# Performance work log

Measured on AMD Instinct MI355X. Metric: run time of the kernel, lower is better.

The kernel has to match this reference:

```python
import jax, jax.numpy as jnp
import numpy as np

N_SLOTS = 64
DECAY = 0.999
B, S, H, M = 4, 4096, 2048, 128


def _l2norm(t, eps=1e-12):
    return t / jnp.maximum(jnp.linalg.norm(t, axis=-1, keepdims=True), eps)


def setup_inputs() -> dict:
    key = jax.random.key(0)
    ks = jax.random.split(key, 6)
    return {
        "x": jax.random.normal(ks[0], (B, S, H), dtype=jnp.float32),
        "W_query": jax.random.normal(ks[1], (M, H), dtype=jnp.float32) * 0.02,
        "W_key": jax.random.normal(ks[2], (M, H), dtype=jnp.float32) * 0.02,
        "W_value": jax.random.normal(ks[3], (M, H), dtype=jnp.float32) * 0.02,
        "W_out": jax.random.normal(ks[4], (H, M), dtype=jnp.float32) * 0.02,
        "W_gate_w": jax.random.normal(ks[5], (1, H), dtype=jnp.float32) * 0.02,
        "W_gate_b": jnp.full((1,), -2.0, dtype=jnp.float32),
        "log_beta": jnp.full((1,), np.log(8.0), dtype=jnp.float32),
        "chunk_size": 64,
    }


def reference(x, W_query, W_key, W_value, W_out, W_gate_w, W_gate_b, log_beta, chunk_size):
    b, s, h = x.shape
    m = W_query.shape[0]
    dt = x.dtype

    q = x @ W_query.T                      # (b, s, m)
    k = _l2norm(x @ W_key.T)               # (b, s, m)
    v = _l2norm(x @ W_value.T)             # (b, s, m)
    gate = jax.nn.sigmoid(x @ W_gate_w.T + W_gate_b)  # (b, s, 1)
    beta = jnp.exp(log_beta).reshape(())

    nc = s // chunk_size
    decay_c = jnp.asarray(DECAY, dt) ** chunk_size

    def chunkify(t):
        # (b, s, d) -> (nc, b, chunk, d)
        return jnp.moveaxis(t.reshape(b, nc, chunk_size, -1), 1, 0)

    qc, kc, vc = chunkify(q), chunkify(k), chunkify(v)
    wc = chunkify(gate)[..., 0]            # (nc, b, chunk)

    K0 = jnp.zeros((N_SLOTS, m), dt)
    V0 = jnp.zeros((N_SLOTS, m), dt)
    s0 = jnp.zeros((N_SLOTS,), dt)
    ptr0 = jnp.asarray(0, jnp.int32)

    def step(carry, inp):
        K_mem, V_mem, mem_strength, ptr = carry
        qch, kch, vch, wch = inp           # (b,c,m) x3, (b,c)
        # --- read: softmax retrieval over active slots ---
        slot_mask = (mem_strength > 1e-8).astype(dt)           # (n_slots,)
        scores = jnp.einsum("bcm,nm->bcn", qch, K_mem) * beta
        scores = scores + (1.0 - slot_mask) * -1e9
        attn = jax.nn.softmax(scores, axis=-1)
        r = jnp.einsum("bcn,nm->bcm", attn, V_mem)
        r = jnp.where(mem_strength.sum() < 1e-8, jnp.zeros_like(r), r)
        # --- write: gated aggregation into one slot ---
        w_sum = jnp.maximum(wch.sum(), 1e-8)
        k_agg = _l2norm((kch * wch[..., None]).sum((0, 1)) / w_sum)
        v_agg = _l2norm((vch * wch[..., None]).sum((0, 1)) / w_sum)
        write_str = wch.mean()
        mem_strength = mem_strength * decay_c
        slot = ptr % N_SLOTS
        K_mem = K_mem.at[slot].set(k_agg)
        V_mem = V_mem.at[slot].set(v_agg)
        mem_strength = mem_strength.at[slot].set(write_str)
        return (K_mem, V_mem, mem_strength, ptr + 1), (r, write_str)

    _, (rs, wss) = jax.lax.scan(step, (K0, V0, s0, ptr0), (qc, kc, vc, wc))

    retrieved = jnp.moveaxis(rs, 0, 1).reshape(b, s, m)
    out = retrieved @ W_out.T              # (b, s, h)
    # clamp output norm to 10
    onorm = jnp.maximum(jnp.linalg.norm(out, axis=-1, keepdims=True), 1e-6)
    out = out * jnp.minimum(10.0 / onorm, 1.0)
    mean_ws = jnp.mean(wss)
    return out, mean_ws
```

## Files before the change

kernel.cpp:

```cpp
#include <hip/hip_runtime.h>
#include <math.h>
#include <stdint.h>

#define NTOK 16384
#define SEQ  4096
#define HD   2048
#define MD   128
#define NCH  64
#define CHK  64

typedef __attribute__((ext_vector_type(8))) _Float16 half8;
typedef __attribute__((ext_vector_type(4))) float floatx4;

__device__ __forceinline__ void gload_lds16(const void* g, void* l) {
    __builtin_amdgcn_global_load_lds(
        (const __attribute__((address_space(1))) unsigned int*)(uintptr_t)g,
        (__attribute__((address_space(3))) unsigned int*)(uintptr_t)l,
        16, 0, 0);
}

__global__ __launch_bounds__(256) void convert_w_kernel(
    const float* __restrict__ Wq, const float* __restrict__ Wk,
    const float* __restrict__ Wv, const float* __restrict__ Wo,
    _Float16* __restrict__ Wcath, _Float16* __restrict__ Woh)
{
    int i = blockIdx.x * 256 + threadIdx.x;
    if (i < 384 * HD) {
        int r = i >> 11;
        float val;
        if (r < 128)      val = Wq[i];
        else if (r < 256) val = Wk[i - 128 * HD];
        else              val = Wv[i - 256 * HD];
        Wcath[i] = (_Float16)val;
    } else {
        int j = i - 384 * HD;
        Woh[j] = (_Float16)Wo[j];
    }
}

__global__ __launch_bounds__(128) void gmat_kernel(
    const float* __restrict__ Wo, float* __restrict__ G)
{
    __shared__ float col[HD];
    int a = blockIdx.x;
    int b = threadIdx.x;
    for (int j = b; j < HD; j += 128) col[j] = Wo[(size_t)j * MD + a];
    __syncthreads();
    float s = 0.f;
    for (int j = 0; j < HD; ++j) s = fmaf(col[j], Wo[(size_t)j * MD + b], s);
    G[a * MD + b] = s;
}

__global__ __launch_bounds__(256, 3) void gemm_proj_mfma(
    const float* __restrict__ x, const _Float16* __restrict__ Wcath,
    const float* __restrict__ Wgw, const float* __restrict__ gb,
    float* __restrict__ q, float* __restrict__ k, float* __restrict__ v,
    float* __restrict__ wg)
{
    __shared__ _Float16 As[2][64 * 64];
    __shared__ _Float16 Bs[2][128 * 64];
    floatx4 acc[2][4];
    #pragma unroll
    for (int i = 0; i < 2; ++i)
        #pragma unroll
        for (int j = 0; j < 4; ++j) acc[i][j] = (floatx4){0.f, 0.f, 0.f, 0.f};

    const int tid  = threadIdx.x;
    const int wave = tid >> 6, lane = tid & 63;
    const int wm = wave & 1, wn = wave >> 1;
    const int row0 = blockIdx.x * 64;
    const int col0 = blockIdx.y * 128;
    const bool do_gate = (blockIdx.y == 0);

    const int ar0 = tid >> 3;
    const int ac0 = (tid & 7) ^ (ar0 & 7);
    const float* xA0 = x + (size_t)(row0 + ar0) * HD + ac0 * 8;
    const float* xA1 = x + (size_t)(row0 + ar0 + 32) * HD + ac0 * 8;
    const float* wgp = Wgw + ac0 * 8;

    float gacc0 = 0.f, gacc1 = 0.f;
    float4 a00, a01, a10, a11, g0, g1;

#define STAGE_B(buf_, k0_) do {                                               \
        _Pragma("unroll")                                                     \
        for (int rnd = 0; rnd < 4; ++rnd) {                                   \
            int sg = rnd * 4 + wave;                                          \
            int br = sg * 8 + (lane >> 3);                                    \
            int bc = (lane & 7) ^ (br & 7);                                   \
            gload_lds16(Wcath + (size_t)(col0 + br) * HD + (k0_) + bc * 8,    \
                        (char*)Bs[buf_] + sg * 1024);                         \
        } } while (0)

#define LOAD_A(k0_) do {                                                      \
        a00 = *(const float4*)(xA0 + (k0_));                                  \
        a01 = *(const float4*)(xA0 + (k0_) + 4);                              \
        a10 = *(const float4*)(xA1 + (k0_));                                  \
        a11 = *(const float4*)(xA1 + (k0_) + 4);                              \
        if (do_gate) {                                                        \
            g0 = *(const float4*)(wgp + (k0_));                               \
            g1 = *(const float4*)(wgp + (k0_) + 4);                           \
        } } while (0)

#define FINISH_A(buf_) do {                                                   \
        if (do_gate) {                                                        \
            gacc0 += a00.x*g0.x + a00.y*g0.y + a00.z*g0.z + a00.w*g0.w        \
                   + a01.x*g1.x + a01.y*g1.y + a01.z*g1.z + a01.w*g1.w;       \
            gacc1 += a10.x*g0.x + a10.y*g0.y + a10.z*g0.z + a10.w*g0.w        \
                   + a11.x*g1.x + a11.y*g1.y + a11.z*g1.z + a11.w*g1.w;       \
        }                                                                     \
        half8 h0, h1;                                                         \
        h0[0] = (_Float16)a00.x; h0[1] = (_Float16)a00.y;                     \
        h0[2] = (_Float16)a00.z; h0[3] = (_Float16)a00.w;                     \
        h0[4] = (_Float16)a01.x; h0[5] = (_Float16)a01.y;                     \
        h0[6] = (_Float16)a01.z; h0[7] = (_Float16)a01.w;                     \
        h1[0] = (_Float16)a10.x; h1[1] = (_Float16)a10.y;                     \
        h1[2] = (_Float16)a10.z; h1[3] = (_Float16)a10.w;                     \
        h1[4] = (_Float16)a11.x; h1[5] = (_Float16)a11.y;                     \
        h1[6] = (_Float16)a11.z; h1[7] = (_Float16)a11.w;                     \
        *(half8*)((char*)As[buf_] + tid * 16)        = h0;                    \
        *(half8*)((char*)As[buf_] + 4096 + tid * 16) = h1;                    \
    } while (0)

#define COMPUTE(buf_) do {                                                    \
        half8 af[2][2], bf[4][2];                                             \
        _Pragma("unroll")                                                     \
        for (int i = 0; i < 2; ++i) {                                         \
            int r  = wm * 32 + i * 16 + (lane & 15);                          \
            int rb = r * 128 + (lane >> 4) * 16;                              \
            int sw = (r & 7) << 4;                                            \
            af[i][0] = *(const half8*)((const char*)As[buf_] + ( rb       ^ sw)); \
            af[i][1] = *(const half8*)((const char*)As[buf_] + ((rb + 64) ^ sw)); \
        }                                                                     \
        _Pragma("unroll")                                                     \
        for (int j = 0; j < 4; ++j) {                                         \
            int r  = wn * 64 + j * 16 + (lane & 15);                          \
            int rb = r * 128 + (lane >> 4) * 16;                              \
            int sw = (r & 7) << 4;                                            \
            bf[j][0] = *(const half8*)((const char*)Bs[buf_] + ( rb       ^ sw)); \
            bf[j][1] = *(const half8*)((const char*)Bs[buf_] + ((rb + 64) ^ sw)); \
        }                                                                     \
        _Pragma("unroll")                                                     \
        for (int ks = 0; ks < 2; ++ks)                                        \
            _Pragma("unroll")                                                 \
            for (int i = 0; i < 2; ++i)                                       \
                _Pragma("unroll")                                             \
                for (int j = 0; j < 4; ++j)                                   \
                    acc[i][j] = __builtin_amdgcn_mfma_f32_16x16x32_f16(       \
                        af[i][ks], bf[j][ks], acc[i][j], 0, 0, 0);            \
    } while (0)

    STAGE_B(0, 0);
    LOAD_A(0);
    FINISH_A(0);
    __syncthreads();

    int cur = 0;
    for (int t = 0; t < HD / 64; ++t) {
        if (t < HD / 64 - 1) {
            STAGE_B(cur ^ 1, (t + 1) * 64);
            LOAD_A((t + 1) * 64);
        }
        COMPUTE(cur);
        if (t < HD / 64 - 1) FINISH_A(cur ^ 1);
        __syncthreads();
        cur ^= 1;
    }

    if (do_gate) {
        gacc0 += __shfl_xor(gacc0, 1);
        gacc0 += __shfl_xor(gacc0, 2);
        gacc0 += __shfl_xor(gacc0, 4);
        gacc1 += __shfl_xor(gacc1, 1);
        gacc1 += __shfl_xor(gacc1, 2);
        gacc1 += __shfl_xor(gacc1, 4);
        if ((tid & 7) == 0) {
            wg[row0 + ar0]      = 1.f / (1.f + expf(-(gacc0 + gb[0])));
            wg[row0 + ar0 + 32] = 1.f / (1.f + expf(-(gacc1 + gb[0])));
        }
    }

    float* dst = (blockIdx.y == 0) ? q : ((blockIdx.y == 1) ? k : v);
    #pragma unroll
    for (int i = 0; i < 2; ++i) {
        int m = row0 + wm * 32 + i * 16 + (lane >> 4) * 4;
        #pragma unroll
        for (int j = 0; j < 4; ++j) {
            int c = wn * 64 + j * 16 + (lane & 15);
            #pragma unroll
            for (int r = 0; r < 4; ++r)
                dst[(size_t)(m + r) * MD + c] = acc[i][j][r];
        }
    }
#undef STAGE_B
#undef LOAD_A
#undef FINISH_A
#undef COMPUTE
}

__global__ __launch_bounds__(256) void normsig_kernel(
    float* __restrict__ k, float* __restrict__ v)
{
    int wave = threadIdx.x >> 6, lane = threadIdx.x & 63;
    int row = blockIdx.x * 4 + wave;
    size_t base = (size_t)row * MD + lane * 2;
    float2 k2 = *reinterpret_cast<float2*>(&k[base]);
    float2 v2 = *reinterpret_cast<float2*>(&v[base]);
    float ks = k2.x * k2.x + k2.y * k2.y;
    float vs = v2.x * v2.x + v2.y * v2.y;
    #pragma unroll
    for (int off = 32; off > 0; off >>= 1) {
        ks += __shfl_xor(ks, off);
        vs += __shfl_xor(vs, off);
    }
    float ki = 1.f / fmaxf(sqrtf(ks), 1e-12f);
    float vi = 1.f / fmaxf(sqrtf(vs), 1e-12f);
    k2.x *= ki; k2.y *= ki; v2.x *= vi; v2.y *= vi;
    *reinterpret_cast<float2*>(&k[base]) = k2;
    *reinterpret_cast<float2*>(&v[base]) = v2;
}

__global__ __launch_bounds__(256) void agg_part_kernel(
    const float* __restrict__ kn, const float* __restrict__ vn,
    const float* __restrict__ w,
    float* __restrict__ kpart, float* __restrict__ vpart,
    float* __restrict__ wpart)
{
    int t = blockIdx.x >> 2, b = blockIdx.x & 3;
    int tid = threadIdx.x;
    int d = tid & 127, h = tid >> 7;
    int base_row = b * SEQ + t * CHK;

    float ka = 0.f, va = 0.f;
    for (int c = h * 32; c < h * 32 + 32; ++c) {
        int row = base_row + c;
        float wv = w[row];
        ka = fmaf(wv, kn[(size_t)row * MD + d], ka);
        va = fmaf(wv, vn[(size_t)row * MD + d], va);
    }
    __shared__ float sk[128], sv[128];
    if (h == 1) { sk[d] = ka; sv[d] = va; }
    __syncthreads();
    if (h == 0) {
        kpart[(size_t)blockIdx.x * 128 + d] = ka + sk[d];
        vpart[(size_t)blockIdx.x * 128 + d] = va + sv[d];
    }
    if (tid < 64) {
        float wv = w[base_row + tid];
        #pragma unroll
        for (int off = 32; off > 0; off >>= 1) wv += __shfl_xor(wv, off);
        if (tid == 0) wpart[blockIdx.x] = wv;
    }
}

__global__ __launch_bounds__(128) void agg_combine_kernel(
    const float* __restrict__ kpart, const float* __restrict__ vpart,
    const float* __restrict__ wpart,
    float* __restrict__ kaT, float* __restrict__ vagg, float* __restrict__ wstr)
{
    int t = blockIdx.x;
    int d = threadIdx.x;
    int wave = d >> 6, lane = d & 63;
    float ku = 0.f, vu = 0.f;
    #pragma unroll
    for (int b = 0; b < 4; ++b) {
        ku += kpart[(size_t)(t * 4 + b) * 128 + d];
        vu += vpart[(size_t)(t * 4 + b) * 128 + d];
    }
    float wsum = wpart[t * 4] + wpart[t * 4 + 1] + wpart[t * 4 + 2] + wpart[t * 4 + 3];
    float winv = 1.f / fmaxf(wsum, 1e-8f);
    ku *= winv; vu *= winv;

    __shared__ float red[4];
    float ks = ku * ku, vs = vu * vu;
    #pragma unroll
    for (int off = 32; off > 0; off >>= 1) {
        ks += __shfl_xor(ks, off);
        vs += __shfl_xor(vs, off);
    }
    if (lane == 0) { red[wave] = ks; red[2 + wave] = vs; }
    __syncthreads();
    float kinv = 1.f / fmaxf(sqrtf(red[0] + red[1]), 1e-12f);
    float vinv = 1.f / fmaxf(sqrtf(red[2] + red[3]), 1e-12f);
    kaT[d * NCH + t] = ku * kinv;
    vagg[t * MD + d] = vu * vinv;
    if (d == 0) wstr[t] = wsum * (1.f / 256.f);
}

__global__ __launch_bounds__(64) void meanws_kernel(
    const float* __restrict__ wstr, float* __restrict__ outp)
{
    int lane = threadIdx.x;
    float v = wstr[lane];
    #pragma unroll
    for (int off = 32; off > 0; off >>= 1) v += __shfl_xor(v, off);
    if (lane == 0) outp[0] = v * (1.f / 64.f);
}

__global__ __launch_bounds__(256) void attn_kernel(
    const float* __restrict__ q, const float* __restrict__ kaT,
    const float* __restrict__ vagg, const float* __restrict__ G,
    const float* __restrict__ logbeta, _Float16* __restrict__ rsh16)
{
    __shared__ float qs[4][128];
    __shared__ float attn_s[4][64];
    __shared__ float rsh[4][128];
    int wave = threadIdx.x >> 6, lane = threadIdx.x & 63;
    int row = blockIdx.x * 4 + wave;
    int t = (row & (SEQ - 1)) >> 6;
    float beta = expf(logbeta[0]);

    qs[wave][lane]      = q[(size_t)row * MD + lane];
    qs[wave][lane + 64] = q[(size_t)row * MD + 64 + lane];
    __syncthreads();

    float sc = -INFINITY;
    if (lane < t) {
        sc = 0.f;
        for (int d = 0; d < 128; ++d)
            sc = fmaf(qs[wave][d], kaT[d * NCH + lane], sc);
        sc *= beta;
    }
    float mx = sc;
    #pragma unroll
    for (int off = 32; off > 0; off >>= 1) mx = fmaxf(mx, __shfl_xor(mx, off));
    float e = (lane < t) ? expf(sc - mx) : 0.f;
    float ssum = e;
    #pragma unroll
    for (int off = 32; off > 0; off >>= 1) ssum += __shfl_xor(ssum, off);
    float attn = (t > 0) ? (e / ssum) : 0.f;
    attn_s[wave][lane] = attn;
    __syncthreads();

    float r0 = 0.f, r1 = 0.f;
    for (int n = 0; n < t; ++n) {
        float a = attn_s[wave][n];
        r0 = fmaf(a, vagg[n * MD + lane], r0);
        r1 = fmaf(a, vagg[n * MD + 64 + lane], r1);
    }
    rsh[wave][lane]      = r0;
    rsh[wave][lane + 64] = r1;
    __syncthreads();

    float t0 = 0.f, t1 = 0.f;
    for (int b = 0; b < 128; ++b) {
        float rb = rsh[wave][b];
        t0 = fmaf(G[b * MD + lane], rb, t0);
        t1 = fmaf(G[b * MD + 64 + lane], rb, t1);
    }
    float quad = r0 * t0 + r1 * t1;
    #pragma unroll
    for (int off = 32; off > 0; off >>= 1) quad += __shfl_xor(quad, off);
    float nrm = fmaxf(sqrtf(fmaxf(quad, 0.f)), 1e-6f);
    float scl = fminf(10.f / nrm, 1.f);
    rsh16[(size_t)row * MD + lane]      = (_Float16)(r0 * scl);
    rsh16[(size_t)row * MD + 64 + lane] = (_Float16)(r1 * scl);
}

__global__ __launch_bounds__(256) void gemm_out_mfma(
    const _Float16* __restrict__ rsh16, const _Float16* __restrict__ Woh,
    float* __restrict__ C)
{
    __shared__ _Float16 As[4096], Bs[4096];
    floatx4 acc[4][4];
    #pragma unroll
    for (int i = 0; i < 4; ++i)
        #pragma unroll
        for (int j = 0; j < 4; ++j) acc[i][j] = (floatx4){0.f, 0.f, 0.f, 0.f};

    const int tid  = threadIdx.x;
    const int wave = tid >> 6, lane = tid & 63;
    const int wm = wave & 1, wn = wave >> 1;
    const int seg_r = lane >> 2;
    const int chunk = lane & 3;
    const int row0 = blockIdx.x * 128;
    const int col0 = blockIdx.y * 128;

    for (int k0 = 0; k0 < MD; k0 += 32) {
        #pragma unroll
        for (int rnd = 0; rnd < 2; ++rnd) {
            int s = wave + 4 * rnd;
            int r = s * 16 + seg_r;
            gload_lds16(rsh16 + (size_t)(row0 + r) * MD + k0 + chunk * 8,
                        As + s * 512);
            gload_lds16(Woh + (size_t)(col0 + r) * MD + k0 + chunk * 8,
                        Bs + s * 512);
        }
        __syncthreads();
        half8 af[4], bf[4];
        #pragma unroll
        for (int i = 0; i < 4; ++i) {
            af[i] = *(const half8*)&As[(wm * 64 + i * 16 + (lane & 15)) * 32 + (lane >> 4) * 8];
            bf[i] = *(const half8*)&Bs[(wn * 64 + i * 16 + (lane & 15)) * 32 + (lane >> 4) * 8];
        }
        #pragma unroll
        for (int i = 0; i < 4; ++i)
            #pragma unroll
            for (int j = 0; j < 4; ++j)
                acc[i][j] = __builtin_amdgcn_mfma_f32_16x16x32_f16(
                    af[i], bf[j], acc[i][j], 0, 0, 0);
        __syncthreads();
    }

    #pragma unroll
    for (int i = 0; i < 4; ++i) {
        int m = row0 + wm * 64 + i * 16 + (lane >> 4) * 4;
        #pragma unroll
        for (int j = 0; j < 4; ++j) {
            int c = col0 + wn * 64 + j * 16 + (lane & 15);
            #pragma unroll
            for (int r = 0; r < 4; ++r)
                C[(size_t)(m + r) * HD + c] = acc[i][j][r];
        }
    }
}

extern "C" void kernel_launch(void* const* d_in, const int* in_sizes, int n_in,
                              void* d_out, int out_size, void* d_ws, size_t ws_size,
                              hipStream_t stream)
{
    const float* x   = (const float*)d_in[0];
    const float* Wq  = (const float*)d_in[1];
    const float* Wk  = (const float*)d_in[2];
    const float* Wv  = (const float*)d_in[3];
    const float* Wo  = (const float*)d_in[4];
    const float* Wgw = (const float*)d_in[5];
    const float* Wgb = (const float*)d_in[6];
    const float* lb  = (const float*)d_in[7];
    float* out = (float*)d_out;

    float* q    = (float*)d_ws;
    float* kn   = q + (size_t)NTOK * MD;
    float* vn   = kn + (size_t)NTOK * MD;
    float* wg   = vn + (size_t)NTOK * MD;
    float* kaT  = wg + NTOK;
    float* vagg = kaT + MD * NCH;
    float* wstr = vagg + NCH * MD;
    float* G    = wstr + 64;
    float* kpart = G + MD * MD;
    float* vpart = kpart + 256 * 128;
    float* wpart = vpart + 256 * 128;
    _Float16* Wcath = (_Float16*)(wpart + 256);
    _Float16* Woh   = Wcath + 384 * HD;
    _Float16* rsh16 = Woh + HD * MD;

    convert_w_kernel<<<dim3(4096), dim3(256), 0, stream>>>(Wq, Wk, Wv, Wo, Wcath, Woh);
    gmat_kernel<<<dim3(128), dim3(128), 0, stream>>>(Wo, G);
    gemm_proj_mfma<<<dim3(NTOK / 64, 3), dim3(256), 0, stream>>>(
        x, Wcath, Wgw, Wgb, q, kn, vn, wg);
    normsig_kernel<<<dim3(NTOK / 4), dim3(256), 0, stream>>>(kn, vn);
    agg_part_kernel<<<dim3(256), dim3(256), 0, stream>>>(kn, vn, wg, kpart, vpart, wpart);
    agg_combine_kernel<<<dim3(NCH), dim3(128), 0, stream>>>(kpart, vpart, wpart, kaT, vagg, wstr);
    meanws_kernel<<<dim3(1), dim3(64), 0, stream>>>(wstr, out + (size_t)NTOK * HD);
    attn_kernel<<<dim3(NTOK / 4), dim3(256), 0, stream>>>(q, kaT, vagg, G, lb, rsh16);
    gemm_out_mfma<<<dim3(NTOK / 128, HD / 128), dim3(256), 0, stream>>>(rsh16, Woh, out);
}
```

Measured before the change: 394.6 us.

## Stage attention constants in LDS and load full-K GEMM tiles with XOR swizzle

The attention kernel now runs 512-thread blocks that each handle 64 rows (one chunk). Each block first copies kaT, vagg and G into shared memory, so the per-row loops read LDS instead of global/L2. The output GEMM loads the full K=128 tile of A and B in one pass with an XOR-swizzled LDS layout, removing the per-k-step barriers and avoiding bank conflicts. The cost is about 114KB of LDS per attention block, which limits it to one block per CU and leaves only 256 blocks. The GEMM's larger 64KB LDS footprint also reduces its occupancy.

Measured after the change: 390.3 us. Within noise of the previous version (-1.1%).

```diff
diff --git a/kernel.cpp b/kernel.cpp
--- a/kernel.cpp
+++ b/kernel.cpp
@@ -296,71 +296,97 @@
     if (lane == 0) outp[0] = v * (1.f / 64.f);
 }
 
-__global__ __launch_bounds__(256) void attn_kernel(
+__global__ __launch_bounds__(512, 1) void attn_kernel(
     const float* __restrict__ q, const float* __restrict__ kaT,
     const float* __restrict__ vagg, const float* __restrict__ G,
     const float* __restrict__ logbeta, _Float16* __restrict__ rsh16)
 {
-    __shared__ float qs[4][128];
-    __shared__ float attn_s[4][64];
-    __shared__ float rsh[4][128];
-    int wave = threadIdx.x >> 6, lane = threadIdx.x & 63;
-    int row = blockIdx.x * 4 + wave;
-    int t = (row & (SEQ - 1)) >> 6;
-    float beta = expf(logbeta[0]);
-
-    qs[wave][lane]      = q[(size_t)row * MD + lane];
-    qs[wave][lane + 64] = q[(size_t)row * MD + 64 + lane];
-    __syncthreads();
-
-    float sc = -INFINITY;
-    if (lane < t) {
-        sc = 0.f;
-        for (int d = 0; d < 128; ++d)
-            sc = fmaf(qs[wave][d], kaT[d * NCH + lane], sc);
-        sc *= beta;
-    }
-    float mx = sc;
-    #pragma unroll
-    for (int off = 32; off > 0; off >>= 1) mx = fmaxf(mx, __shfl_xor(mx, off));
-    float e = (lane < t) ? expf(sc - mx) : 0.f;
-    float ssum = e;
-    #pragma unroll
-    for (int off = 32; off > 0; off >>= 1) ssum += __shfl_xor(ssum, off);
-    float attn = (t > 0) ? (e / ssum) : 0.f;
-    attn_s[wave][lane] = attn;
-    __syncthreads();
-
-    float r0 = 0.f, r1 = 0.f;
-    for (int n = 0; n < t; ++n) {
-        float a = attn_s[wave][n];
-        r0 = fmaf(a, vagg[n * MD + lane], r0);
-        r1 = fmaf(a, vagg[n * MD + 64 + lane], r1);
-    }
-    rsh[wave][lane]      = r0;
-    rsh[wave][lane + 64] = r1;
-    __syncthreads();
-
-    float t0 = 0.f, t1 = 0.f;
-    for (int b = 0; b < 128; ++b) {
-        float rb = rsh[wave][b];
-        t0 = fmaf(G[b * MD + lane], rb, t0);
-        t1 = fmaf(G[b * MD + 64 + lane], rb, t1);
-    }
-    float quad = r0 * t0 + r1 * t1;
-    #pragma unroll
-    for (int off = 32; off > 0; off >>= 1) quad += __shfl_xor(quad, off);
-    float nrm = fmaxf(sqrtf(fmaxf(quad, 0.f)), 1e-6f);
-    float scl = fminf(10.f / nrm, 1.f);
-    rsh16[(size_t)row * MD + lane]      = (_Float16)(r0 * scl);
-    rsh16[(size_t)row * MD + 64 + lane] = (_Float16)(r1 * scl);
+    __shared__ float kaT_s[MD * NCH];
+    __shared__ float vagg_s[NCH * MD];
+    __shared__ float G_s[MD * MD];
+    __shared__ float qs[8][MD];
+    __shared__ float attn_sh[8][64];
+    __shared__ float rsh_sh[8][MD];
+
+    const int tid  = threadIdx.x;
+    const int wave = tid >> 6, lane = tid & 63;
+    const int row0 = blockIdx.x * 64;
+    const int t = (row0 & (SEQ - 1)) >> 6;
+    const float beta = expf(logbeta[0]);
+
+    {
+        const float4* s0 = (const float4*)kaT;
+        const float4* s1 = (const float4*)vagg;
+        const float4* s2 = (const float4*)G;
+        float4* d0 = (float4*)kaT_s;
+        float4* d1 = (float4*)vagg_s;
+        float4* d2 = (float4*)G_s;
+        #pragma unroll
+        for (int i = 0; i < 4; ++i) {
+            d0[tid + i * 512] = s0[tid + i * 512];
+            d1[tid + i * 512] = s1[tid + i * 512];
+        }
+        #pragma unroll
+        for (int i = 0; i < 8; ++i)
+            d2[tid + i * 512] = s2[tid + i * 512];
+    }
+    __syncthreads();
+
+    for (int rr = 0; rr < 8; ++rr) {
+        const int row = row0 + wave * 8 + rr;
+        float q0 = q[(size_t)row * MD + lane];
+        float q1 = q[(size_t)row * MD + 64 + lane];
+        qs[wave][lane]      = q0;
+        qs[wave][lane + 64] = q1;
+
+        float sc = -INFINITY;
+        if (lane < t) {
+            sc = 0.f;
+            for (int d = 0; d < 128; ++d)
+                sc = fmaf(qs[wave][d], kaT_s[d * NCH + lane], sc);
+            sc *= beta;
+        }
+        float mx = sc;
+        #pragma unroll
+        for (int off = 32; off > 0; off >>= 1) mx = fmaxf(mx, __shfl_xor(mx, off));
+        float e = (lane < t) ? expf(sc - mx) : 0.f;
+        float ssum = e;
+        #pragma unroll
+        for (int off = 32; off > 0; off >>= 1) ssum += __shfl_xor(ssum, off);
+        float attn = (t > 0) ? (e / ssum) : 0.f;
+        attn_sh[wave][lane] = attn;
+
+        float r0 = 0.f, r1 = 0.f;
+        for (int n = 0; n < t; ++n) {
+            float a = attn_sh[wave][n];
+            r0 = fmaf(a, vagg_s[n * MD + lane], r0);
+            r1 = fmaf(a, vagg_s[n * MD + 64 + lane], r1);
+        }
+        rsh_sh[wave][lane]      = r0;
+        rsh_sh[wave][lane + 64] = r1;
+
+        float t0 = 0.f, t1 = 0.f;
+        for (int b = 0; b < 128; ++b) {
+            float rb = rsh_sh[wave][b];
+            t0 = fmaf(G_s[b * MD + lane], rb, t0);
+            t1 = fmaf(G_s[b * MD + 64 + lane], rb, t1);
+        }
+        float quad = r0 * t0 + r1 * t1;
+        #pragma unroll
+        for (int off = 32; off > 0; off >>= 1) quad += __shfl_xor(quad, off);
+        float nrm = fmaxf(sqrtf(fmaxf(quad, 0.f)), 1e-6f);
+        float scl = fminf(10.f / nrm, 1.f);
+        rsh16[(size_t)row * MD + lane]      = (_Float16)(r0 * scl);
+        rsh16[(size_t)row * MD + 64 + lane] = (_Float16)(r1 * scl);
+    }
 }
 
 __global__ __launch_bounds__(256) void gemm_out_mfma(
     const _Float16* __restrict__ rsh16, const _Float16* __restrict__ Woh,
     float* __restrict__ C)
 {
-    __shared__ _Float16 As[4096], Bs[4096];
+    __shared__ _Float16 As[128 * 128];
+    __shared__ _Float16 Bs[128 * 128];
     floatx4 acc[4][4];
     #pragma unroll
     for (int i = 0; i < 4; ++i)
@@ -370,27 +396,37 @@
     const int tid  = threadIdx.x;
     const int wave = tid >> 6, lane = tid & 63;
     const int wm = wave & 1, wn = wave >> 1;
-    const int seg_r = lane >> 2;
-    const int chunk = lane & 3;
     const int row0 = blockIdx.x * 128;
     const int col0 = blockIdx.y * 128;
 
-    for (int k0 = 0; k0 < MD; k0 += 32) {
-        #pragma unroll
-        for (int rnd = 0; rnd < 2; ++rnd) {
-            int s = wave + 4 * rnd;
-            int r = s * 16 + seg_r;
-            gload_lds16(rsh16 + (size_t)(row0 + r) * MD + k0 + chunk * 8,
-                        As + s * 512);
-            gload_lds16(Woh + (size_t)(col0 + r) * MD + k0 + chunk * 8,
-                        Bs + s * 512);
-        }
-        __syncthreads();
+    const int sr = lane >> 4;
+    const int sp = lane & 15;
+    #pragma unroll
+    for (int rnd = 0; rnd < 8; ++rnd) {
+        int seg = wave * 8 + rnd;
+        int r = seg * 4 + sr;
+        int c = sp ^ (r & 15);
+        gload_lds16(rsh16 + (size_t)(row0 + r) * MD + c * 8,
+                    (char*)As + seg * 1024);
+        gload_lds16(Woh + (size_t)(col0 + r) * MD + c * 8,
+                    (char*)Bs + seg * 1024);
+    }
+    __syncthreads();
+
+    #pragma unroll
+    for (int kf = 0; kf < 4; ++kf) {
         half8 af[4], bf[4];
         #pragma unroll
         for (int i = 0; i < 4; ++i) {
-            af[i] = *(const half8*)&As[(wm * 64 + i * 16 + (lane & 15)) * 32 + (lane >> 4) * 8];
-            bf[i] = *(const half8*)&Bs[(wn * 64 + i * 16 + (lane & 15)) * 32 + (lane >> 4) * 8];
+            int r = wm * 64 + i * 16 + (lane & 15);
+            int g = kf * 4 + (lane >> 4);
+            af[i] = *(const half8*)((const char*)As + r * 256 + ((g ^ (r & 15)) * 16));
+        }
+        #pragma unroll
+        for (int j = 0; j < 4; ++j) {
+            int r = wn * 64 + j * 16 + (lane & 15);
+            int g = kf * 4 + (lane >> 4);
+            bf[j] = *(const half8*)((const char*)Bs + r * 256 + ((g ^ (r & 15)) * 16));
         }
         #pragma unroll
         for (int i = 0; i < 4; ++i)
@@ -398,7 +434,6 @@
             for (int j = 0; j < 4; ++j)
                 acc[i][j] = __builtin_amdgcn_mfma_f32_16x16x32_f16(
                     af[i], bf[j], acc[i][j], 0, 0, 0);
-        __syncthreads();
     }
 
     #pragma unroll
@@ -451,6 +486,6 @@
     agg_part_kernel<<<dim3(256), dim3(256), 0, stream>>>(kn, vn, wg, kpart, vpart, wpart);
     agg_combine_kernel<<<dim3(NCH), dim3(128), 0, stream>>>(kpart, vpart, wpart, kaT, vagg, wstr);
     meanws_kernel<<<dim3(1), dim3(64), 0, stream>>>(wstr, out + (size_t)NTOK * HD);
-    attn_kernel<<<dim3(NTOK / 4), dim3(256), 0, stream>>>(q, kaT, vagg, G, lb, rsh16);
+    attn_kernel<<<dim3(NTOK / 64), dim3(512), 0, stream>>>(q, kaT, vagg, G, lb, rsh16);
     gemm_out_mfma<<<dim3(NTOK / 128, HD / 128), dim3(256), 0, stream>>>(rsh16, Woh, out);
 }
```
